# Performance work log

Hardware: AMD Instinct MI355X
Metric: run time of the kernel (lower is better)

The kernel has to match this reference:

```python
import jax, jax.numpy as jnp
from jax import lax
import numpy as np

CODEBOOK_SIZE = 512
VQ_DIM = 32


def _conv(x, w, b):
    # NCHW conv, 3x3, stride 1, SAME padding (padding=1 in torch)
    y = lax.conv_general_dilated(x, w, (1, 1), 'SAME',
                                 dimension_numbers=('NCHW', 'OIHW', 'NCHW'))
    return y + b[None, :, None, None]


def _maxpool2(x):
    return lax.reduce_window(x, -jnp.inf, lax.max, (1, 1, 2, 2), (1, 1, 2, 2), 'VALID')


def _upsample2(x):
    return jnp.repeat(jnp.repeat(x, 2, axis=2), 2, axis=3)


def _vq(x_flat, codebook):
    # x_flat: [b, n, d]; codebook: [K, d]
    # squared euclidean distances via expansion (avoids [b,n,K,d] tensor)
    x2 = jnp.sum(x_flat * x_flat, axis=-1, keepdims=True)          # [b,n,1]
    c2 = jnp.sum(codebook * codebook, axis=-1)                     # [K]
    xc = jnp.einsum('bnd,kd->bnk', x_flat, codebook)               # [b,n,K]
    dist = x2 - 2.0 * xc + c2[None, None, :]
    indices = jnp.argmin(dist, axis=-1)                            # [b,n] int
    quantized = codebook[indices]                                  # [b,n,d]
    # commitment loss (codebook treated as non-grad target, EMA-style)
    commit_loss = jnp.mean((jax.lax.stop_gradient(quantized) - x_flat) ** 2)
    # straight-through estimator
    quantized = x_flat + jax.lax.stop_gradient(quantized - x_flat)
    return quantized, indices, commit_loss


def _forward(x, w1, b1, w2, b2, codebook, w3, b3, w4, b4):
    h = _conv(x, w1, b1)            # [b,16,256,256]
    h = _maxpool2(h)                # [b,16,128,128]
    h = jax.nn.gelu(h, approximate=False)
    h = _conv(h, w2, b2)            # [b,32,128,128]
    h = _maxpool2(h)                # [b,32,64,64]
    b, c, H, W = h.shape
    h_flat = jnp.transpose(h, (0, 2, 3, 1)).reshape(b, H * W, c)   # b (h w) c
    q, indices, commit_loss = _vq(h_flat, codebook)
    h = jnp.transpose(q.reshape(b, H, W, c), (0, 3, 1, 2))         # [b,32,64,64]
    h = _upsample2(h)               # [b,32,128,128]
    h = _conv(h, w3, b3)            # [b,16,128,128]
    h = jax.nn.gelu(h, approximate=False)
    h = _upsample2(h)               # [b,16,256,256]
    h = _conv(h, w4, b4)            # [b,1,256,256]
    return jnp.clip(h, -1.0, 1.0), indices, commit_loss


def setup_inputs() -> dict:
    key = jax.random.key(0)
    ks = jax.random.split(key, 10)
    def w(k, shape):
        fan_in = int(np.prod(shape[1:]))
        return jax.random.normal(k, shape, dtype=jnp.float32) * (1.0 / np.sqrt(fan_in))
    return {
        'x': jax.random.normal(ks[0], (64, 1, 256, 256), dtype=jnp.float32),
        'w1': w(ks[1], (16, 1, 3, 3)),  'b1': jnp.zeros((16,), jnp.float32),
        'w2': w(ks[2], (32, 16, 3, 3)), 'b2': jnp.zeros((32,), jnp.float32),
        'codebook': jax.random.normal(ks[3], (CODEBOOK_SIZE, VQ_DIM), dtype=jnp.float32),
        'w3': w(ks[4], (16, 32, 3, 3)), 'b3': jnp.zeros((16,), jnp.float32),
        'w4': w(ks[5], (1, 16, 3, 3)),  'b4': jnp.zeros((1,), jnp.float32),
    }


def reference(x, w1, b1, w2, b2, codebook, w3, b3, w4, b4):
    return _forward(x, w1, b1, w2, b2, codebook, w3, b3, w4, b4)
```

## Files before the change

### kernel.cpp

```cpp
#include <hip/hip_runtime.h>
#include <math.h>


#define GELUF(v) (0.5f * (v) * (1.0f + erff((v) * 0.70710678118654752440f)))
#define MAXFLAG 262144

typedef __attribute__((ext_vector_type(8))) short short8;
typedef __attribute__((ext_vector_type(4))) float float4v;

static __device__ inline unsigned short f2bf(float f) {
    unsigned u = __float_as_uint(f);
    unsigned r = (u + 0x7FFFu + ((u >> 16) & 1u)) >> 16;
    return (unsigned short)r;
}
static __device__ inline float bf2f(unsigned short h) {
    return __uint_as_float(((unsigned)h) << 16);
}

__global__ __launch_bounds__(256) void k_enc(const float* __restrict__ x,
                                             const float* __restrict__ w1,
                                             const float* __restrict__ b1,
                                             const unsigned short* __restrict__ w2h,
                                             const unsigned short* __restrict__ w2l,
                                             const float* __restrict__ b2,
                                             float* __restrict__ h2) {
    __shared__ __align__(16) float s_scratch[2048];
    __shared__ __align__(16) unsigned short s_hi[18 * 2 * 18 * 8];
    __shared__ __align__(16) unsigned short s_lo[18 * 2 * 18 * 8];

    int tid = threadIdx.x;
    int n = blockIdx.x >> 6;
    int tile = blockIdx.x & 63;
    int cx0 = (tile & 7) << 4, cy0 = (tile >> 3) << 4;

    {
        const float* xin = x + (size_t)n * 65536;
        int gy0 = 2 * cy0 - 3, gx0 = 2 * cx0 - 3;
        for (int e = tid; e < 1444; e += 256) {
            int r = e / 38, c = e - r * 38;
            int gy = gy0 + r, gx = gx0 + c;
            float v = 0.0f;
            if (gy >= 0 && gy < 256 && gx >= 0 && gx < 256) v = xin[gy * 256 + gx];
            s_scratch[r * 40 + c] = v;
        }
    }
    __syncthreads();

    for (int e = tid; e < 324; e += 256) {
        int r = e / 18, c = e - r * 18;
        int hy = cy0 - 1 + r, hx = cx0 - 1 + c;
        uint ph[8], pl[8];
        if (hy >= 0 && hy < 128 && hx >= 0 && hx < 128) {
            float patch[4][4];
            const float* sp = s_scratch + (2 * r) * 40 + 2 * c;
#pragma unroll
            for (int i = 0; i < 4; i++)
#pragma unroll
                for (int j = 0; j < 4; j++)
                    patch[i][j] = sp[i * 40 + j];
            unsigned short hi[16], lo[16];
#pragma unroll
            for (int ch = 0; ch < 16; ch++) {
                float m = -INFINITY;
#pragma unroll
                for (int sy = 0; sy < 2; sy++)
#pragma unroll
                    for (int sx = 0; sx < 2; sx++) {
                        float acc = b1[ch];
#pragma unroll
                        for (int ky = 0; ky < 3; ky++)
#pragma unroll
                            for (int kx = 0; kx < 3; kx++)
                                acc += w1[ch * 9 + ky * 3 + kx] * patch[sy + ky][sx + kx];
                        m = fmaxf(m, acc);
                    }
                float g = GELUF(m);
                hi[ch] = f2bf(g);
                lo[ch] = f2bf(g - bf2f(hi[ch]));
            }
#pragma unroll
            for (int dw = 0; dw < 8; dw++) {
                ph[dw] = (uint)hi[2 * dw] | ((uint)hi[2 * dw + 1] << 16);
                pl[dw] = (uint)lo[2 * dw] | ((uint)lo[2 * dw + 1] << 16);
            }
        } else {
#pragma unroll
            for (int dw = 0; dw < 8; dw++) { ph[dw] = 0; pl[dw] = 0; }
        }
        ((uint4*)s_hi)[(r * 2) * 18 + c]     = make_uint4(ph[0], ph[1], ph[2], ph[3]);
        ((uint4*)s_hi)[(r * 2 + 1) * 18 + c] = make_uint4(ph[4], ph[5], ph[6], ph[7]);
        ((uint4*)s_lo)[(r * 2) * 18 + c]     = make_uint4(pl[0], pl[1], pl[2], pl[3]);
        ((uint4*)s_lo)[(r * 2 + 1) * 18 + c] = make_uint4(pl[4], pl[5], pl[6], pl[7]);
    }
    __syncthreads();

    int lane = tid & 63, wid = tid >> 6;
    int m = lane & 15, quad = lane >> 4;
    int tl = quad >> 1, half = quad & 1;

    float4v acc[4][2];
#pragma unroll
    for (int mt = 0; mt < 4; mt++)
#pragma unroll
        for (int nt = 0; nt < 2; nt++)
            acc[mt][nt] = (float4v){0.0f, 0.0f, 0.0f, 0.0f};

    for (int s = 0; s < 5; s++) {
        int tA = (s < 4) ? (2 * s + tl) : 8;
        int tB = (s < 4) ? (2 * s + tl) : (8 + tl);
        short8 Bh[2], Bl[2];
#pragma unroll
        for (int nt = 0; nt < 2; nt++) {
            int u = ((nt * 16 + m) * 10 + tB) * 2 + half;
            Bh[nt] = *(const short8*)(w2h + (u << 3));
            Bl[nt] = *(const short8*)(w2l + (u << 3));
        }
        int ky = tA / 3, kx = tA - 3 * (tA / 3);
        short8 Ah[4], Al[4];
#pragma unroll
        for (int mt = 0; mt < 4; mt++) {
            int u = (((wid * 4 + mt + ky) * 2 + half) * 18) + m + kx;
            Ah[mt] = *(const short8*)(s_hi + (u << 3));
            Al[mt] = *(const short8*)(s_lo + (u << 3));
        }
#pragma unroll
        for (int mt = 0; mt < 4; mt++)
#pragma unroll
            for (int nt = 0; nt < 2; nt++) {
                float4v z = acc[mt][nt];
                z = __builtin_amdgcn_mfma_f32_16x16x32_bf16(Al[mt], Bh[nt], z, 0, 0, 0);
                z = __builtin_amdgcn_mfma_f32_16x16x32_bf16(Ah[mt], Bl[nt], z, 0, 0, 0);
                z = __builtin_amdgcn_mfma_f32_16x16x32_bf16(Ah[mt], Bh[nt], z, 0, 0, 0);
                acc[mt][nt] = z;
            }
    }

    float* s_pool = s_scratch;
#pragma unroll
    for (int nt = 0; nt < 2; nt++) {
        int cout = nt * 16 + m;
        float bias = b2[cout];
#pragma unroll
        for (int mtp = 0; mtp < 2; mtp++) {
            float4v a0 = acc[2 * mtp][nt], a1 = acc[2 * mtp + 1][nt];
            float p0 = fmaxf(fmaxf(a0[0], a0[1]), fmaxf(a1[0], a1[1])) + bias;
            float p1 = fmaxf(fmaxf(a0[2], a0[3]), fmaxf(a1[2], a1[3])) + bias;
            int py = wid * 2 + mtp;
            int px = quad * 2;
            s_pool[cout * 64 + py * 8 + px]     = p0;
            s_pool[cout * 64 + py * 8 + px + 1] = p1;
        }
    }
    __syncthreads();
    {
        int c = tid >> 3, pr = tid & 7;
        float* dst = h2 + (((size_t)(n * 32 + c)) << 12) + ((cy0 >> 1) + pr) * 64 + (cx0 >> 1);
        const float4* src = (const float4*)(s_pool + c * 64 + pr * 8);
        ((float4*)dst)[0] = src[0];
        ((float4*)dst)[1] = src[1];
    }
}

__global__ __launch_bounds__(256) void k_vq_mfma(const float* __restrict__ h2,
                                                 const unsigned short* __restrict__ cbh,
                                                 const unsigned short* __restrict__ cbl,
                                                 const float* __restrict__ c2g,
                                                 float* __restrict__ idx_out,
                                                 float* __restrict__ loss_out,
                                                 int* __restrict__ nflag,
                                                 int* __restrict__ flags) {
    __shared__ float s_best[256], s_best2[256];
    __shared__ int   s_bi[256];
    __shared__ float wsum[4];

    int tid = threadIdx.x;
    int lane = tid & 63;
    int wid  = tid >> 6;
    int m    = lane & 15;
    int quad = lane >> 4;

    int img = blockIdx.x >> 4;
    int sp0 = (blockIdx.x & 15) << 8;
    const float* xb = h2 + ((size_t)(img * 32) << 12) + sp0;

    short8 Ahi[4], Alo[4];
    float x2r[4][4];
    float x2own[4];
#pragma unroll
    for (int mt = 0; mt < 4; mt++) {
        const float* xp = xb + wid * 64 + mt * 16 + m;
        float x2 = 0.0f;
#pragma unroll
        for (int j = 0; j < 8; j++) {
            float fe = xp[(size_t)(quad * 8 + j) << 12];
            x2 += fe * fe;
            unsigned short hi = f2bf(fe);
            unsigned short lo = f2bf(fe - bf2f(hi));
            Ahi[mt][j] = (short)hi;
            Alo[mt][j] = (short)lo;
        }
        x2 += __shfl_xor(x2, 16);
        x2 += __shfl_xor(x2, 32);
        x2own[mt] = x2;
    }
#pragma unroll
    for (int mt = 0; mt < 4; mt++)
#pragma unroll
        for (int r = 0; r < 4; r++)
            x2r[mt][r] = __shfl(x2own[mt], quad * 4 + r);

    float best[4][4], best2[4][4];
    int bi[4][4];
#pragma unroll
    for (int mt = 0; mt < 4; mt++)
#pragma unroll
        for (int r = 0; r < 4; r++) {
            best[mt][r] = INFINITY; best2[mt][r] = INFINITY; bi[mt][r] = 0;
        }

    size_t boff = ((size_t)m << 5) + (quad << 3);
    short8 Bh = *(const short8*)(cbh + boff);
    short8 Bl = *(const short8*)(cbl + boff);
    float  c2v = c2g[m];

    for (int nt = 0; nt < 32; nt++) {
        short8 curBh = Bh, curBl = Bl;
        float  curc2 = c2v;
        if (nt < 31) {
            size_t o = boff + ((size_t)(nt + 1) << 9);
            Bh = *(const short8*)(cbh + o);
            Bl = *(const short8*)(cbl + o);
            c2v = c2g[(nt + 1) * 16 + m];
        }
        int ncode = nt * 16 + m;

        float4v acc[4];
#pragma unroll
        for (int mt = 0; mt < 4; mt++) {
            float4v z = {0.0f, 0.0f, 0.0f, 0.0f};
            z = __builtin_amdgcn_mfma_f32_16x16x32_bf16(Alo[mt], curBh, z, 0, 0, 0);
            z = __builtin_amdgcn_mfma_f32_16x16x32_bf16(Ahi[mt], curBl, z, 0, 0, 0);
            z = __builtin_amdgcn_mfma_f32_16x16x32_bf16(Ahi[mt], curBh, z, 0, 0, 0);
            acc[mt] = z;
        }
#pragma unroll
        for (int mt = 0; mt < 4; mt++)
#pragma unroll
            for (int r = 0; r < 4; r++) {
                float dist = fmaf(acc[mt][r], -2.0f, curc2);
                best2[mt][r] = fminf(best2[mt][r], fmaxf(dist, best[mt][r]));
                bool lt = dist < best[mt][r];
                bi[mt][r] = lt ? ncode : bi[mt][r];
                best[mt][r] = fminf(best[mt][r], dist);
            }
    }

#pragma unroll
    for (int mt = 0; mt < 4; mt++)
#pragma unroll
        for (int r = 0; r < 4; r++) {
            float b1v = best[mt][r], b2v = best2[mt][r];
            int   biv = bi[mt][r];
#pragma unroll
            for (int mask = 1; mask < 16; mask <<= 1) {
                float ob = __shfl_xor(b1v, mask);
                float ob2 = __shfl_xor(b2v, mask);
                int   obi = __shfl_xor(biv, mask);
                b2v = fminf(fminf(b2v, ob2), fmaxf(b1v, ob));
                if (ob < b1v || (ob == b1v && obi < biv)) { b1v = ob; biv = obi; }
            }
            if (m == 0) {
                int p = wid * 64 + mt * 16 + quad * 4 + r;
                s_best[p] = b1v + x2r[mt][r];
                s_best2[p] = b2v + x2r[mt][r];
                s_bi[p] = biv;
            }
        }
    __syncthreads();

    int pos = blockIdx.x * 256 + tid;
    float bb = s_best[tid], bb2 = s_best2[tid];
    int   kk = s_bi[tid];
    idx_out[pos] = (float)kk;

    float eps = 0.02f + 0.0005f * fabsf(bb);
    if (bb2 - bb < eps) {
        int slot = atomicAdd(nflag, 1);
        if (slot < MAXFLAG) flags[slot] = pos;
    }

    float lsum = fmaxf(bb, 0.0f);
#pragma unroll
    for (int o = 32; o > 0; o >>= 1) lsum += __shfl_down(lsum, o);
    if (lane == 0) wsum[wid] = lsum;
    __syncthreads();
    if (tid == 0)
        atomicAdd(loss_out, (wsum[0] + wsum[1] + wsum[2] + wsum[3]) * (1.0f / 8388608.0f));
}

__global__ __launch_bounds__(256) void k_lut(const float* __restrict__ wc3,
                                             const float* __restrict__ cb,
                                             float* __restrict__ lut) {
    int code = blockIdx.x;
    int t = threadIdx.x;
    float s = 0.0f;
    if (code < 512) {
        int pp = t >> 6, rem = t & 63;
        const float* wp = wc3 + pp * 2048 + rem;
        const float* cr = cb + code * 32;
        for (int cin = 0; cin < 32; cin++)
            s += wp[cin * 64] * cr[cin];
    }
    lut[(size_t)code * 256 + t] = s;
}

__global__ __launch_bounds__(64) void k_repair(const float* __restrict__ x,
                                               const float* __restrict__ w1,
                                               const float* __restrict__ b1,
                                               const float* __restrict__ w2,
                                               const float* __restrict__ b2,
                                               const float* __restrict__ cb,
                                               float* __restrict__ idx_out,
                                               const int* __restrict__ nflag,
                                               const int* __restrict__ flags) {
    __shared__ double h1w[16][16];
    __shared__ double xvd[32];
    int lane = threadIdx.x;
    int cnt = *nflag;
    if (cnt > MAXFLAG) cnt = MAXFLAG;

    for (int fi = blockIdx.x; fi < cnt; fi += gridDim.x) {
        int pos = flags[fi];
        int n = pos >> 12, sp = pos & 4095, yo = sp >> 6, xo = sp & 63;

        int pix = lane >> 2, cg = lane & 3;
        int dy = pix >> 2, dx = pix & 3;
        int yh = 2 * yo - 1 + dy, xh = 2 * xo - 1 + dx;
        double hv[4] = {0.0, 0.0, 0.0, 0.0};
        if (yh >= 0 && yh < 128 && xh >= 0 && xh < 128) {
            const float* xin = x + (size_t)n * 65536;
            double patch[4][4];
            int y0 = 2 * yh - 1, x0 = 2 * xh - 1;
#pragma unroll
            for (int i = 0; i < 4; i++) {
                int iy = y0 + i;
                bool oy = (iy >= 0 && iy < 256);
#pragma unroll
                for (int j = 0; j < 4; j++) {
                    int ix = x0 + j;
                    patch[i][j] = (oy && ix >= 0 && ix < 256) ? (double)xin[iy * 256 + ix] : 0.0;
                }
            }
#pragma unroll
            for (int j = 0; j < 4; j++) {
                int c = cg * 4 + j;
                double mm = -INFINITY;
#pragma unroll
                for (int sy = 0; sy < 2; sy++)
#pragma unroll
                    for (int sx = 0; sx < 2; sx++) {
                        double acc = (double)b1[c];
#pragma unroll
                        for (int ky = 0; ky < 3; ky++)
#pragma unroll
                            for (int kx = 0; kx < 3; kx++)
                                acc += (double)w1[c * 9 + ky * 3 + kx] * patch[sy + ky][sx + kx];
                        mm = fmax(mm, acc);
                    }
                hv[j] = 0.5 * mm * (1.0 + erf(mm * 0.70710678118654752440));
            }
        }
        __syncthreads();
#pragma unroll
        for (int j = 0; j < 4; j++) h1w[cg * 4 + j][pix] = hv[j];
        __syncthreads();

        if (lane < 32) {
            double bb = (double)b2[lane];
            double acc[2][2] = {{bb, bb}, {bb, bb}};
            for (int cin = 0; cin < 16; cin++)
#pragma unroll
                for (int ky = 0; ky < 3; ky++)
#pragma unroll
                    for (int kx = 0; kx < 3; kx++) {
                        double wv = (double)w2[((lane * 16 + cin) * 3 + ky) * 3 + kx];
#pragma unroll
                        for (int sy = 0; sy < 2; sy++)
#pragma unroll
                            for (int sx = 0; sx < 2; sx++)
                                acc[sy][sx] += wv * h1w[cin][(sy + ky) * 4 + (sx + kx)];
                    }
            xvd[lane] = fmax(fmax(acc[0][0], acc[0][1]), fmax(acc[1][0], acc[1][1]));
        }
        __syncthreads();

        double x2 = 0.0;
        for (int d = 0; d < 32; d++) x2 += xvd[d] * xvd[d];
        double best = INFINITY;
        int bi = 0;
        for (int j = 0; j < 8; j++) {
            int k = lane * 8 + j;
            const float* cp = cb + k * 32;
            double c2 = 0.0, dot = 0.0;
#pragma unroll
            for (int d = 0; d < 32; d++) {
                double cd = (double)cp[d];
                c2 += cd * cd;
                dot += xvd[d] * cd;
            }
            double dist = x2 - 2.0 * dot + c2;
            if (dist < best) { best = dist; bi = k; }
        }
#pragma unroll
        for (int o = 32; o > 0; o >>= 1) {
            double od = __shfl_down(best, o);
            int oi = __shfl_down(bi, o);
            if (od < best || (od == best && oi < bi)) { best = od; bi = oi; }
        }
        bi = __shfl(bi, 0);

        if (lane == 0) idx_out[(size_t)n * 4096 + sp] = (float)bi;
    }
}

__global__ __launch_bounds__(256) void k_prep(const float* __restrict__ w2,
                                              const float* __restrict__ w3,
                                              const float* __restrict__ w4,
                                              const float* __restrict__ cb,
                                              unsigned short* __restrict__ w2h,
                                              unsigned short* __restrict__ w2l,
                                              float* __restrict__ wc3,
                                              float* __restrict__ wc4,
                                              unsigned short* __restrict__ cbh,
                                              unsigned short* __restrict__ cbl,
                                              float* __restrict__ c2g) {
    const int masks[2][2] = {{1, 6}, {3, 4}};
    for (int e = threadIdx.x; e < 8192; e += 256) {
        int cout = e & 15, tap = (e >> 4) & 3, cin = (e >> 6) & 31, pp = e >> 11;
        int rm = masks[pp >> 1][tap >> 1], cm = masks[pp & 1][tap & 1];
        float s = 0.0f;
        for (int ky = 0; ky < 3; ky++)
            if ((rm >> ky) & 1)
                for (int kx = 0; kx < 3; kx++)
                    if ((cm >> kx) & 1) s += w3[(cout * 32 + cin) * 9 + ky * 3 + kx];
        wc3[e] = s;
    }
    for (int e = threadIdx.x; e < 1024; e += 256) {
        int tap = e & 3, cin = (e >> 2) & 15, pp = e >> 6;
        int rm = masks[pp >> 1][tap >> 1], cm = masks[pp & 1][tap & 1];
        float s = 0.0f;
        for (int ky = 0; ky < 3; ky++)
            if ((rm >> ky) & 1)
                for (int kx = 0; kx < 3; kx++)
                    if ((cm >> kx) & 1) s += w4[cin * 9 + ky * 3 + kx];
        wc4[e] = s;
    }
    for (int e = threadIdx.x; e < 5120; e += 256) {
        int cout = e / 160;
        int rem = e - cout * 160;
        int tap = rem >> 4;
        int cin = rem & 15;
        float v = 0.0f;
        if (tap < 9) {
            int ky = tap / 3, kx = tap - 3 * (tap / 3);
            v = w2[((cout * 16 + cin) * 3 + ky) * 3 + kx];
        }
        unsigned short hi = f2bf(v);
        unsigned short lo = f2bf(v - bf2f(hi));
        w2h[e] = hi;
        w2l[e] = lo;
    }
    for (int e = threadIdx.x; e < 16384; e += 256) {
        float v = cb[e];
        unsigned short hi = f2bf(v);
        cbh[e] = hi;
        cbl[e] = f2bf(v - bf2f(hi));
    }
    for (int k = threadIdx.x; k < 512; k += 256) {
        float c2 = 0.0f;
#pragma unroll
        for (int d = 0; d < 32; d++) {
            float fe = cb[k * 32 + d];
            c2 += fe * fe;
        }
        c2g[k] = c2;
    }
}

__global__ __launch_bounds__(256) void k_dec(const float* __restrict__ idxf,
                                             const float* __restrict__ lut,
                                             const float* __restrict__ b3,
                                             const float* __restrict__ wc4,
                                             const float* __restrict__ b4,
                                             float* __restrict__ out) {
    __shared__ int   s_code[11 * 11];
    __shared__ float s_h3[16 * 324];

    int tid = threadIdx.x;
    int n = blockIdx.x >> 6;
    int tile = blockIdx.x & 63;
    int ty = tile >> 3, tx = tile & 7;

    if (tid < 121) {
        int row = tid / 11, col = tid - row * 11;
        int ca = 8 * ty - 1 + row, cbx = 8 * tx - 1 + col;
        int code = 512;
        if (ca >= 0 && ca < 64 && cbx >= 0 && cbx < 64)
            code = (int)idxf[((size_t)n << 12) + (ca << 6) + cbx];
        s_code[tid] = code;
    }
    __syncthreads();

    for (int e = tid; e < 324; e += 256) {
        int r = e / 18, cc = e - r * 18;
        int Y = 16 * ty - 1 + r, X = 16 * tx - 1 + cc;
        float hv[16];
        if (Y >= 0 && Y < 128 && X >= 0 && X < 128) {
            int pp = ((Y & 1) << 1) | (X & 1);
            int la0 = (Y >> 1) - 1 + (Y & 1) - (8 * ty - 1);
            int lb0 = (X >> 1) - 1 + (X & 1) - (8 * tx - 1);
            float acc[16];
#pragma unroll
            for (int c = 0; c < 16; c++) acc[c] = b3[c];
#pragma unroll
            for (int dy = 0; dy < 2; dy++)
#pragma unroll
                for (int dx = 0; dx < 2; dx++) {
                    int code = s_code[(la0 + dy) * 11 + lb0 + dx];
                    const float4* lp = (const float4*)(lut + (size_t)code * 256 +
                                                       pp * 64 + (dy * 2 + dx) * 16);
#pragma unroll
                    for (int j = 0; j < 4; j++) {
                        float4 w = lp[j];
                        acc[4 * j + 0] += w.x;
                        acc[4 * j + 1] += w.y;
                        acc[4 * j + 2] += w.z;
                        acc[4 * j + 3] += w.w;
                    }
                }
#pragma unroll
            for (int c = 0; c < 16; c++) hv[c] = GELUF(acc[c]);
        } else {
#pragma unroll
            for (int c = 0; c < 16; c++) hv[c] = 0.0f;
        }
#pragma unroll
        for (int c = 0; c < 16; c++) s_h3[c * 324 + e] = hv[c];
    }
    __syncthreads();

    int ly = tid >> 4, lx = tid & 15;
    float bv = b4[0];
    float acc2[2][2] = {{bv, bv}, {bv, bv}};
    for (int cin = 0; cin < 16; cin++) {
        const float* hc = s_h3 + cin * 324;
        float v[3][3];
#pragma unroll
        for (int r = 0; r < 3; r++)
#pragma unroll
            for (int cc = 0; cc < 3; cc++)
                v[r][cc] = hc[(ly + r) * 18 + lx + cc];
#pragma unroll
        for (int py = 0; py < 2; py++)
#pragma unroll
            for (int px = 0; px < 2; px++)
#pragma unroll
                for (int dy = 0; dy < 2; dy++)
#pragma unroll
                    for (int dx = 0; dx < 2; dx++)
                        acc2[py][px] += wc4[(py * 2 + px) * 64 + cin * 4 + dy * 2 + dx] *
                                        v[py + dy][px + dx];
    }
    int a = 16 * ty + ly, b = 16 * tx + lx;
#pragma unroll
    for (int py = 0; py < 2; py++) {
        float2 f2 = make_float2(fminf(fmaxf(acc2[py][0], -1.0f), 1.0f),
                                fminf(fmaxf(acc2[py][1], -1.0f), 1.0f));
        *(float2*)(out + (size_t)n * 65536 + (2 * a + py) * 256 + 2 * b) = f2;
    }
}

extern "C" void kernel_launch(void* const* d_in, const int* in_sizes, int n_in,
                              void* d_out, int out_size, void* d_ws, size_t ws_size,
                              hipStream_t stream) {
    const float* x  = (const float*)d_in[0];
    const float* w1 = (const float*)d_in[1];
    const float* b1 = (const float*)d_in[2];
    const float* w2 = (const float*)d_in[3];
    const float* b2 = (const float*)d_in[4];
    const float* cb = (const float*)d_in[5];
    const float* w3 = (const float*)d_in[6];
    const float* b3 = (const float*)d_in[7];
    const float* w4 = (const float*)d_in[8];
    const float* b4 = (const float*)d_in[9];

    float* out      = (float*)d_out;
    float* idx_out  = out + 4194304;
    float* loss_out = out + 4194304 + 262144;

    char* ws = (char*)d_ws;
    float* h2  = (float*)(ws + (size_t)67108864);
    float* lut = (float*)(ws + (size_t)67108864);
    size_t T = 100663296;
    float* wc3 = (float*)(ws + T);
    float* wc4 = (float*)(ws + T + 32768);
    unsigned short* w2h = (unsigned short*)(ws + T + 36864);
    unsigned short* w2l = (unsigned short*)(ws + T + 47104);
    int* nflag = (int*)(ws + T + 57344);
    int* flags = (int*)(ws + T + 57408);
    size_t T2 = T + 57408 + 1048576;
    unsigned short* cbh = (unsigned short*)(ws + T2);
    unsigned short* cbl = (unsigned short*)(ws + T2 + 32768);
    float* c2g = (float*)(ws + T2 + 65536);

    (void)hipMemsetAsync(loss_out, 0, 4, stream);
    (void)hipMemsetAsync(nflag, 0, 4, stream);

    k_prep<<<1, 256, 0, stream>>>(w2, w3, w4, cb, w2h, w2l, wc3, wc4, cbh, cbl, c2g);
    k_enc<<<4096, 256, 0, stream>>>(x, w1, b1, w2h, w2l, b2, h2);
    k_vq_mfma<<<1024, 256, 0, stream>>>(h2, cbh, cbl, c2g, idx_out, loss_out, nflag, flags);
    k_lut<<<513, 256, 0, stream>>>(wc3, cb, lut);
    k_repair<<<16384, 64, 0, stream>>>(x, w1, b1, w2, b2, cb, idx_out, nflag, flags);
    k_dec<<<4096, 256, 0, stream>>>(idx_out, lut, b3, wc4, b4, out);
}
```

Measured before the change: 384.2 us.

## Fuse VQ nearest-code search into encoder kernel, dropping h2 round trip

The encoder kernel now runs the codebook distance search directly on its pooled 8x8x32 tile held in shared memory, instead of writing h2 to global memory and launching a separate VQ kernel. This removes a 32 MB write and read plus one launch. In exchange, each encoder block now scans the whole 512-entry codebook for only 64 positions, one MFMA M-tile per wave. Codebook reuse per block drops and the loss atomics grow from 1024 to 4096. Shared-memory padding (stride 65) was added to avoid bank conflicts on the transposed reads.

```diff
diff --git a/kernel.cpp b/kernel.cpp
--- a/kernel.cpp
+++ b/kernel.cpp
@@ -23,10 +23,18 @@
                                              const unsigned short* __restrict__ w2h,
                                              const unsigned short* __restrict__ w2l,
                                              const float* __restrict__ b2,
-                                             float* __restrict__ h2) {
-    __shared__ __align__(16) float s_scratch[2048];
+                                             const unsigned short* __restrict__ cbh,
+                                             const unsigned short* __restrict__ cbl,
+                                             const float* __restrict__ c2g,
+                                             float* __restrict__ idx_out,
+                                             float* __restrict__ loss_out,
+                                             int* __restrict__ nflag,
+                                             int* __restrict__ flags) {
+    __shared__ __align__(16) float s_scratch[2112];
     __shared__ __align__(16) unsigned short s_hi[18 * 2 * 18 * 8];
     __shared__ __align__(16) unsigned short s_lo[18 * 2 * 18 * 8];
+    __shared__ float s_best[64], s_best2[64];
+    __shared__ int   s_bi[64];
 
     int tid = threadIdx.x;
     int n = blockIdx.x >> 6;
@@ -136,6 +144,7 @@
     }
 
     float* s_pool = s_scratch;
+    __syncthreads();
 #pragma unroll
     for (int nt = 0; nt < 2; nt++) {
         int cout = nt * 16 + m;
@@ -147,76 +156,33 @@
             float p1 = fmaxf(fmaxf(a0[2], a0[3]), fmaxf(a1[2], a1[3])) + bias;
             int py = wid * 2 + mtp;
             int px = quad * 2;
-            s_pool[cout * 64 + py * 8 + px]     = p0;
-            s_pool[cout * 64 + py * 8 + px + 1] = p1;
-        }
-    }
-    __syncthreads();
-    {
-        int c = tid >> 3, pr = tid & 7;
-        float* dst = h2 + (((size_t)(n * 32 + c)) << 12) + ((cy0 >> 1) + pr) * 64 + (cx0 >> 1);
-        const float4* src = (const float4*)(s_pool + c * 64 + pr * 8);
-        ((float4*)dst)[0] = src[0];
-        ((float4*)dst)[1] = src[1];
-    }
-}
-
-__global__ __launch_bounds__(256) void k_vq_mfma(const float* __restrict__ h2,
-                                                 const unsigned short* __restrict__ cbh,
-                                                 const unsigned short* __restrict__ cbl,
-                                                 const float* __restrict__ c2g,
-                                                 float* __restrict__ idx_out,
-                                                 float* __restrict__ loss_out,
-                                                 int* __restrict__ nflag,
-                                                 int* __restrict__ flags) {
-    __shared__ float s_best[256], s_best2[256];
-    __shared__ int   s_bi[256];
-    __shared__ float wsum[4];
-
-    int tid = threadIdx.x;
-    int lane = tid & 63;
-    int wid  = tid >> 6;
-    int m    = lane & 15;
-    int quad = lane >> 4;
-
-    int img = blockIdx.x >> 4;
-    int sp0 = (blockIdx.x & 15) << 8;
-    const float* xb = h2 + ((size_t)(img * 32) << 12) + sp0;
-
-    short8 Ahi[4], Alo[4];
-    float x2r[4][4];
-    float x2own[4];
-#pragma unroll
-    for (int mt = 0; mt < 4; mt++) {
-        const float* xp = xb + wid * 64 + mt * 16 + m;
-        float x2 = 0.0f;
-#pragma unroll
-        for (int j = 0; j < 8; j++) {
-            float fe = xp[(size_t)(quad * 8 + j) << 12];
-            x2 += fe * fe;
-            unsigned short hi = f2bf(fe);
-            unsigned short lo = f2bf(fe - bf2f(hi));
-            Ahi[mt][j] = (short)hi;
-            Alo[mt][j] = (short)lo;
-        }
-        x2 += __shfl_xor(x2, 16);
-        x2 += __shfl_xor(x2, 32);
-        x2own[mt] = x2;
-    }
-#pragma unroll
-    for (int mt = 0; mt < 4; mt++)
-#pragma unroll
-        for (int r = 0; r < 4; r++)
-            x2r[mt][r] = __shfl(x2own[mt], quad * 4 + r);
-
-    float best[4][4], best2[4][4];
-    int bi[4][4];
-#pragma unroll
-    for (int mt = 0; mt < 4; mt++)
-#pragma unroll
-        for (int r = 0; r < 4; r++) {
-            best[mt][r] = INFINITY; best2[mt][r] = INFINITY; bi[mt][r] = 0;
-        }
+            s_pool[cout * 65 + py * 8 + px]     = p0;
+            s_pool[cout * 65 + py * 8 + px + 1] = p1;
+        }
+    }
+    __syncthreads();
+
+    int pbase = wid * 16;
+    short8 Ahi, Alo;
+    float x2own = 0.0f;
+#pragma unroll
+    for (int j = 0; j < 8; j++) {
+        float fe = s_pool[(quad * 8 + j) * 65 + pbase + m];
+        x2own += fe * fe;
+        unsigned short hi = f2bf(fe);
+        Ahi[j] = (short)hi;
+        Alo[j] = (short)f2bf(fe - bf2f(hi));
+    }
+    x2own += __shfl_xor(x2own, 16);
+    x2own += __shfl_xor(x2own, 32);
+    float x2r[4];
+#pragma unroll
+    for (int r = 0; r < 4; r++) x2r[r] = __shfl(x2own, quad * 4 + r);
+
+    float best[4], best2[4];
+    int bi[4];
+#pragma unroll
+    for (int r = 0; r < 4; r++) { best[r] = INFINITY; best2[r] = INFINITY; bi[r] = 0; }
 
     size_t boff = ((size_t)m << 5) + (quad << 3);
     short8 Bh = *(const short8*)(cbh + boff);
@@ -234,68 +200,59 @@
         }
         int ncode = nt * 16 + m;
 
-        float4v acc[4];
-#pragma unroll
-        for (int mt = 0; mt < 4; mt++) {
-            float4v z = {0.0f, 0.0f, 0.0f, 0.0f};
-            z = __builtin_amdgcn_mfma_f32_16x16x32_bf16(Alo[mt], curBh, z, 0, 0, 0);
-            z = __builtin_amdgcn_mfma_f32_16x16x32_bf16(Ahi[mt], curBl, z, 0, 0, 0);
-            z = __builtin_amdgcn_mfma_f32_16x16x32_bf16(Ahi[mt], curBh, z, 0, 0, 0);
-            acc[mt] = z;
-        }
-#pragma unroll
-        for (int mt = 0; mt < 4; mt++)
-#pragma unroll
-            for (int r = 0; r < 4; r++) {
-                float dist = fmaf(acc[mt][r], -2.0f, curc2);
-                best2[mt][r] = fminf(best2[mt][r], fmaxf(dist, best[mt][r]));
-                bool lt = dist < best[mt][r];
-                bi[mt][r] = lt ? ncode : bi[mt][r];
-                best[mt][r] = fminf(best[mt][r], dist);
-            }
-    }
-
-#pragma unroll
-    for (int mt = 0; mt < 4; mt++)
+        float4v z = {0.0f, 0.0f, 0.0f, 0.0f};
+        z = __builtin_amdgcn_mfma_f32_16x16x32_bf16(Alo, curBh, z, 0, 0, 0);
+        z = __builtin_amdgcn_mfma_f32_16x16x32_bf16(Ahi, curBl, z, 0, 0, 0);
+        z = __builtin_amdgcn_mfma_f32_16x16x32_bf16(Ahi, curBh, z, 0, 0, 0);
 #pragma unroll
         for (int r = 0; r < 4; r++) {
-            float b1v = best[mt][r], b2v = best2[mt][r];
-            int   biv = bi[mt][r];
-#pragma unroll
-            for (int mask = 1; mask < 16; mask <<= 1) {
-                float ob = __shfl_xor(b1v, mask);
-                float ob2 = __shfl_xor(b2v, mask);
-                int   obi = __shfl_xor(biv, mask);
-                b2v = fminf(fminf(b2v, ob2), fmaxf(b1v, ob));
-                if (ob < b1v || (ob == b1v && obi < biv)) { b1v = ob; biv = obi; }
-            }
-            if (m == 0) {
-                int p = wid * 64 + mt * 16 + quad * 4 + r;
-                s_best[p] = b1v + x2r[mt][r];
-                s_best2[p] = b2v + x2r[mt][r];
-                s_bi[p] = biv;
-            }
-        }
-    __syncthreads();
-
-    int pos = blockIdx.x * 256 + tid;
-    float bb = s_best[tid], bb2 = s_best2[tid];
-    int   kk = s_bi[tid];
-    idx_out[pos] = (float)kk;
-
-    float eps = 0.02f + 0.0005f * fabsf(bb);
-    if (bb2 - bb < eps) {
-        int slot = atomicAdd(nflag, 1);
-        if (slot < MAXFLAG) flags[slot] = pos;
-    }
-
-    float lsum = fmaxf(bb, 0.0f);
-#pragma unroll
-    for (int o = 32; o > 0; o >>= 1) lsum += __shfl_down(lsum, o);
-    if (lane == 0) wsum[wid] = lsum;
-    __syncthreads();
-    if (tid == 0)
-        atomicAdd(loss_out, (wsum[0] + wsum[1] + wsum[2] + wsum[3]) * (1.0f / 8388608.0f));
+            float dist = fmaf(z[r], -2.0f, curc2);
+            best2[r] = fminf(best2[r], fmaxf(dist, best[r]));
+            bool lt = dist < best[r];
+            bi[r] = lt ? ncode : bi[r];
+            best[r] = fminf(best[r], dist);
+        }
+    }
+
+#pragma unroll
+    for (int r = 0; r < 4; r++) {
+        float b1v = best[r], b2v = best2[r];
+        int   biv = bi[r];
+#pragma unroll
+        for (int mask = 1; mask < 16; mask <<= 1) {
+            float ob = __shfl_xor(b1v, mask);
+            float ob2 = __shfl_xor(b2v, mask);
+            int   obi = __shfl_xor(biv, mask);
+            b2v = fminf(fminf(b2v, ob2), fmaxf(b1v, ob));
+            if (ob < b1v || (ob == b1v && obi < biv)) { b1v = ob; biv = obi; }
+        }
+        if (m == 0) {
+            int p = pbase + quad * 4 + r;
+            s_best[p] = b1v + x2r[r];
+            s_best2[p] = b2v + x2r[r];
+            s_bi[p] = biv;
+        }
+    }
+    __syncthreads();
+
+    if (tid < 64) {
+        float bb = s_best[tid], bb2 = s_best2[tid];
+        int   kk = s_bi[tid];
+        int py = tid >> 3, px = tid & 7;
+        int sp = ((cy0 >> 1) + py) * 64 + (cx0 >> 1) + px;
+        idx_out[(size_t)n * 4096 + sp] = (float)kk;
+
+        float eps = 0.02f + 0.0005f * fabsf(bb);
+        if (bb2 - bb < eps) {
+            int slot = atomicAdd(nflag, 1);
+            if (slot < MAXFLAG) flags[slot] = (n << 12) + sp;
+        }
+
+        float lsum = fmaxf(bb, 0.0f);
+#pragma unroll
+        for (int o = 32; o > 0; o >>= 1) lsum += __shfl_down(lsum, o);
+        if (tid == 0) atomicAdd(loss_out, lsum * (1.0f / 8388608.0f));
+    }
 }
 
 __global__ __launch_bounds__(256) void k_lut(const float* __restrict__ wc3,
@@ -599,7 +556,6 @@
     float* loss_out = out + 4194304 + 262144;
 
     char* ws = (char*)d_ws;
-    float* h2  = (float*)(ws + (size_t)67108864);
     float* lut = (float*)(ws + (size_t)67108864);
     size_t T = 100663296;
     float* wc3 = (float*)(ws + T);
@@ -617,8 +573,8 @@
     (void)hipMemsetAsync(nflag, 0, 4, stream);
 
     k_prep<<<1, 256, 0, stream>>>(w2, w3, w4, cb, w2h, w2l, wc3, wc4, cbh, cbl, c2g);
-    k_enc<<<4096, 256, 0, stream>>>(x, w1, b1, w2h, w2l, b2, h2);
-    k_vq_mfma<<<1024, 256, 0, stream>>>(h2, cbh, cbl, c2g, idx_out, loss_out, nflag, flags);
+    k_enc<<<4096, 256, 0, stream>>>(x, w1, b1, w2h, w2l, b2, cbh, cbl, c2g,
+                                    idx_out, loss_out, nflag, flags);
     k_lut<<<513, 256, 0, stream>>>(wc3, cb, lut);
     k_repair<<<16384, 64, 0, stream>>>(x, w1, b1, w2, b2, cb, idx_out, nflag, flags);
     k_dec<<<4096, 256, 0, stream>>>(idx_out, lut, b3, wc4, b4, out);
```

Result: no change. 380.5 us (-1.0%).
